# Performance work log

Measured on AMD Instinct MI355X. Metric: run time of the kernel, lower is better.

Reference implementation:

```python
import jax, jax.numpy as jnp
import numpy as np

N = 1_000_000
D = 128          # p + q, with p = q = 64
C = 1024         # number of classes
LAMBDA_LC = 1.0
LAMBDA_CC = 1.0
LAMBDA_SB = 1.0
LC_EPSILON = 0.1


def setup_inputs() -> dict:
    key = jax.random.key(0)
    k1, k2 = jax.random.split(key)
    z = jax.random.normal(k1, (N, D), dtype=jnp.float32)
    labels = jax.random.randint(k2, (N,), 0, C, dtype=jnp.int64)
    # metric vector J: +1 on first p dims, -1 on last q dims
    J = jnp.concatenate([jnp.ones(D // 2, jnp.float32), -jnp.ones(D // 2, jnp.float32)])
    return {"z": z, "labels": labels, "J": J}


def reference(z, labels, J):
    # q_J(z) = sum_d J_d z_d^2 ; shape (N,)
    q = jnp.sum(z * z * J, axis=-1)

    # light-cone penalty: mean(relu(eps - |q|))
    lc = jnp.mean(jax.nn.relu(LC_EPSILON - jnp.abs(q)))

    # causal consistency: mean over classes of within-class variance of q
    # (segment-sum form of the torch one-hot scatter; identical math)
    labels32 = labels.astype(jnp.int32)
    count = jnp.clip(jax.ops.segment_sum(jnp.ones_like(q), labels32, num_segments=C), 1.0)
    cls_mean = jax.ops.segment_sum(q, labels32, num_segments=C) / count
    sq_dev = (q - cls_mean[labels32]) ** 2
    cls_var = jax.ops.segment_sum(sq_dev, labels32, num_segments=C) / count
    cc = jnp.mean(cls_var)

    # signature balance: (mean q)^2
    sb = jnp.mean(q) ** 2

    return LAMBDA_LC * lc + LAMBDA_CC * cc + LAMBDA_SB * sb
```

## Files before the change

kernel.cpp:

```cpp
#include <hip/hip_runtime.h>

#define D_CONST 128
#define C_CONST 1024
#define LC_EPS  0.1f

#define G_HIST   512
#define TPB      1024
#define WAVES_PB (TPB / 64)
#define RED_TPB  G_HIST

#define P_OFF    0
#define LCQ_OFF  (G_HIST * 3 * C_CONST)
#define VARS_OFF (LCQ_OFF + 2 * G_HIST)
#define MAIN_WS_FLOATS (VARS_OFF + C_CONST)

__global__ __launch_bounds__(TPB) void qstat_main(const float* __restrict__ z,
                                                  const int* __restrict__ labels,
                                                  float* __restrict__ ws,
                                                  int n) {
    __shared__ float h[3 * C_CONST];
    __shared__ float wred[2 * WAVES_PB];

    for (int i = threadIdx.x; i < 3 * C_CONST; i += TPB) h[i] = 0.0f;
    __syncthreads();

    const int lane = threadIdx.x & 63;
    const int wv   = threadIdx.x >> 6;
    const int gw   = blockIdx.x * WAVES_PB + wv;
    const int nw   = G_HIST * WAVES_PB;
    const int half = lane >> 5;
    const int sub  = lane & 31;
    const float sign = (sub < 16) ? 1.0f : -1.0f;

    float lc_acc = 0.0f;
    float q_acc  = 0.0f;

    const int n_pairs = n >> 1;

    for (int base = gw * 2; base < n_pairs; base += nw * 2) {
        const int pair1 = base + 1;
        const bool has1 = pair1 < n_pairs;

        const int row0 = base * 2 + half;
        const float4 v0 = ((const float4*)(z + (long long)row0 * D_CONST))[sub];
        float4 v1;
        int row1 = 0;
        if (has1) {
            row1 = pair1 * 2 + half;
            v1 = ((const float4*)(z + (long long)row1 * D_CONST))[sub];
        }

        float s0 = (v0.x * v0.x + v0.y * v0.y + v0.z * v0.z + v0.w * v0.w) * sign;
        s0 += __shfl_xor(s0, 1);
        s0 += __shfl_xor(s0, 2);
        s0 += __shfl_xor(s0, 4);
        s0 += __shfl_xor(s0, 8);
        s0 += __shfl_xor(s0, 16);
        if (sub == 0) {
            const float q = s0;
            lc_acc += fmaxf(LC_EPS - fabsf(q), 0.0f);
            q_acc  += q;
            const int c = labels[row0];
            atomicAdd(&h[c], 1.0f);
            atomicAdd(&h[C_CONST + c], q);
            atomicAdd(&h[2 * C_CONST + c], q * q);
        }

        if (has1) {
            float s1 = (v1.x * v1.x + v1.y * v1.y + v1.z * v1.z + v1.w * v1.w) * sign;
            s1 += __shfl_xor(s1, 1);
            s1 += __shfl_xor(s1, 2);
            s1 += __shfl_xor(s1, 4);
            s1 += __shfl_xor(s1, 8);
            s1 += __shfl_xor(s1, 16);
            if (sub == 0) {
                const float q = s1;
                lc_acc += fmaxf(LC_EPS - fabsf(q), 0.0f);
                q_acc  += q;
                const int c = labels[row1];
                atomicAdd(&h[c], 1.0f);
                atomicAdd(&h[C_CONST + c], q);
                atomicAdd(&h[2 * C_CONST + c], q * q);
            }
        }
    }

    lc_acc += __shfl_xor(lc_acc, 32);
    q_acc  += __shfl_xor(q_acc, 32);
    if (lane == 0) { wred[wv] = lc_acc; wred[WAVES_PB + wv] = q_acc; }
    __syncthreads();

    if (threadIdx.x == 0) {
        float l = 0.0f, q = 0.0f;
        for (int i = 0; i < WAVES_PB; i++) { l += wred[i]; q += wred[WAVES_PB + i]; }
        ws[LCQ_OFF + blockIdx.x * 2]     = l;
        ws[LCQ_OFF + blockIdx.x * 2 + 1] = q;
    }

    float* dst = ws + P_OFF + (long long)blockIdx.x * 3 * C_CONST;
    for (int i = threadIdx.x; i < 3 * C_CONST; i += TPB) dst[i] = h[i];
}

__global__ __launch_bounds__(RED_TPB) void reduce_classes(const float* __restrict__ ws,
                                                          float* __restrict__ vars) {
    const int c = blockIdx.x;
    const int g = threadIdx.x;
    const float* p = ws + P_OFF + (long long)g * 3 * C_CONST;
    float cnt = p[c];
    float s   = p[C_CONST + c];
    float s2  = p[2 * C_CONST + c];

    for (int m = 1; m < 64; m <<= 1) {
        cnt += __shfl_xor(cnt, m);
        s   += __shfl_xor(s, m);
        s2  += __shfl_xor(s2, m);
    }
    __shared__ float r[3][RED_TPB / 64];
    const int wv = threadIdx.x >> 6;
    if ((threadIdx.x & 63) == 0) { r[0][wv] = cnt; r[1][wv] = s; r[2][wv] = s2; }
    __syncthreads();
    if (threadIdx.x == 0) {
        float C0 = 0, S0 = 0, S20 = 0;
        for (int i = 0; i < RED_TPB / 64; i++) { C0 += r[0][i]; S0 += r[1][i]; S20 += r[2][i]; }
        const float cc = fmaxf(C0, 1.0f);
        vars[c] = (S20 - S0 * S0 / cc) / cc;
    }
}

__global__ __launch_bounds__(C_CONST) void final_scalar(const float* __restrict__ ws,
                                                        float* __restrict__ out,
                                                        int n) {
    __shared__ float red[C_CONST];
    __shared__ float red2[2 * G_HIST];
    const int t = threadIdx.x;
    red[t] = ws[VARS_OFF + t];
    if (t < G_HIST) {
        red2[t]          = ws[LCQ_OFF + t * 2];
        red2[G_HIST + t] = ws[LCQ_OFF + t * 2 + 1];
    }
    __syncthreads();
    for (int off = C_CONST / 2; off > 0; off >>= 1) {
        if (t < off) red[t] += red[t + off];
        if (off <= G_HIST / 2 && t < off) {
            red2[t] += red2[t + off];
            red2[G_HIST + t] += red2[G_HIST + t + off];
        }
        __syncthreads();
    }
    if (t == 0) {
        const float lc = red2[0] / (float)n;
        const float mq = red2[G_HIST] / (float)n;
        out[0] = lc + red[0] / (float)C_CONST + mq * mq;
    }
}

#define FB_WS_FLOATS (3 * C_CONST + 2)

__global__ __launch_bounds__(256) void qstat_fb(const float* __restrict__ z,
                                                const int* __restrict__ labels,
                                                float* __restrict__ ws,
                                                int n) {
    const int lane = threadIdx.x & 63;
    const long long gw = (long long)blockIdx.x * 4 + (threadIdx.x >> 6);
    const long long nw = (long long)gridDim.x * 4;
    const int half = lane >> 5, sub = lane & 31;
    const float sign = (sub < 16) ? 1.0f : -1.0f;
    float lc = 0.0f, qa = 0.0f;
    const long long n_pairs = (long long)n >> 1;
    for (long long pair = gw; pair < n_pairs; pair += nw) {
        const long long row = pair * 2 + half;
        float4 v = ((const float4*)(z + row * D_CONST))[sub];
        float s = (v.x * v.x + v.y * v.y + v.z * v.z + v.w * v.w) * sign;
        s += __shfl_xor(s, 1); s += __shfl_xor(s, 2); s += __shfl_xor(s, 4);
        s += __shfl_xor(s, 8); s += __shfl_xor(s, 16);
        if (sub == 0) {
            lc += fmaxf(LC_EPS - fabsf(s), 0.0f); qa += s;
            const int c = labels[row];
            atomicAdd(&ws[c], 1.0f);
            atomicAdd(&ws[C_CONST + c], s);
            atomicAdd(&ws[2 * C_CONST + c], s * s);
        }
    }
    lc += __shfl_xor(lc, 32); qa += __shfl_xor(qa, 32);
    if (lane == 0) {
        atomicAdd(&ws[3 * C_CONST], lc);
        atomicAdd(&ws[3 * C_CONST + 1], qa);
    }
}

__global__ __launch_bounds__(C_CONST) void finalize_fb(const float* __restrict__ ws,
                                                       float* __restrict__ out, int n) {
    __shared__ float red[C_CONST];
    const int c = threadIdx.x;
    const float cnt = fmaxf(ws[c], 1.0f);
    const float s = ws[C_CONST + c], s2 = ws[2 * C_CONST + c];
    red[c] = (s2 - s * s / cnt) / cnt;
    __syncthreads();
    for (int off = C_CONST / 2; off > 0; off >>= 1) {
        if (c < off) red[c] += red[c + off];
        __syncthreads();
    }
    if (c == 0) {
        out[0] = ws[3 * C_CONST] / (float)n + red[0] / (float)C_CONST
               + (ws[3 * C_CONST + 1] / (float)n) * (ws[3 * C_CONST + 1] / (float)n);
    }
}

extern "C" void kernel_launch(void* const* d_in, const int* in_sizes, int n_in,
                              void* d_out, int out_size, void* d_ws, size_t ws_size,
                              hipStream_t stream) {
    const float* z      = (const float*)d_in[0];
    const int*   labels = (const int*)d_in[1];
    float* ws  = (float*)d_ws;
    float* out = (float*)d_out;
    const int n = in_sizes[1];

    if (ws_size >= (size_t)MAIN_WS_FLOATS * sizeof(float)) {
        qstat_main<<<G_HIST, TPB, 0, stream>>>(z, labels, ws, n);
        reduce_classes<<<C_CONST, RED_TPB, 0, stream>>>(ws, ws + VARS_OFF);
        final_scalar<<<1, C_CONST, 0, stream>>>(ws, out, n);
    } else {
        hipMemsetAsync(ws, 0, FB_WS_FLOATS * sizeof(float), stream);
        qstat_fb<<<2048, 256, 0, stream>>>(z, labels, ws, n);
        finalize_fb<<<1, C_CONST, 0, stream>>>(ws, out, n);
    }
}
```

Before: 665.5 us.

## Transpose partial histograms, fuse final reduction via last-block atomics, nontemporal loads

Partial per-block histograms are now stored class-major, so the class reduction kernel reads contiguous memory instead of strided, uncoalesced loads. The final scalar kernel is folded into the reduction kernel using atomic accumulation and a last-block-done counter, which removes one launch. Loads of z become nontemporal to avoid polluting the cache. The transposed store in the main kernel is now strided, and the fused finish relies on ws accumulators being zeroed by block 0 of the preceding kernel.

```diff
diff --git a/kernel.cpp b/kernel.cpp
--- a/kernel.cpp
+++ b/kernel.cpp
@@ -7,19 +7,23 @@
 #define G_HIST   512
 #define TPB      1024
 #define WAVES_PB (TPB / 64)
-#define RED_TPB  G_HIST
+#define RED_TPB  512
+
+typedef float f32x4 __attribute__((ext_vector_type(4)));
 
 #define P_OFF    0
-#define LCQ_OFF  (G_HIST * 3 * C_CONST)
-#define VARS_OFF (LCQ_OFF + 2 * G_HIST)
-#define MAIN_WS_FLOATS (VARS_OFF + C_CONST)
-
-__global__ __launch_bounds__(TPB) void qstat_main(const float* __restrict__ z,
-                                                  const int* __restrict__ labels,
-                                                  float* __restrict__ ws,
-                                                  int n) {
+#define LCQ_OFF  (3 * C_CONST * G_HIST)
+#define ACC_OFF  (LCQ_OFF + 2 * G_HIST)
+#define MAIN_WS_FLOATS (ACC_OFF + 4)
+
+__global__ __launch_bounds__(TPB, 8) void qstat_main(const float* __restrict__ z,
+                                                     const int* __restrict__ labels,
+                                                     float* __restrict__ ws,
+                                                     int n) {
     __shared__ float h[3 * C_CONST];
     __shared__ float wred[2 * WAVES_PB];
+
+    if (blockIdx.x == 0 && threadIdx.x < 4) ws[ACC_OFF + threadIdx.x] = 0.0f;
 
     for (int i = threadIdx.x; i < 3 * C_CONST; i += TPB) h[i] = 0.0f;
     __syncthreads();
@@ -42,12 +46,14 @@
         const bool has1 = pair1 < n_pairs;
 
         const int row0 = base * 2 + half;
-        const float4 v0 = ((const float4*)(z + (long long)row0 * D_CONST))[sub];
-        float4 v1;
+        const f32x4* zp0 = (const f32x4*)(z + (long long)row0 * D_CONST);
+        const f32x4 v0 = __builtin_nontemporal_load(zp0 + sub);
+        f32x4 v1;
         int row1 = 0;
         if (has1) {
             row1 = pair1 * 2 + half;
-            v1 = ((const float4*)(z + (long long)row1 * D_CONST))[sub];
+            const f32x4* zp1 = (const f32x4*)(z + (long long)row1 * D_CONST);
+            v1 = __builtin_nontemporal_load(zp1 + sub);
         }
 
         float s0 = (v0.x * v0.x + v0.y * v0.y + v0.z * v0.z + v0.w * v0.w) * sign;
@@ -93,64 +99,64 @@
     if (threadIdx.x == 0) {
         float l = 0.0f, q = 0.0f;
         for (int i = 0; i < WAVES_PB; i++) { l += wred[i]; q += wred[WAVES_PB + i]; }
-        ws[LCQ_OFF + blockIdx.x * 2]     = l;
-        ws[LCQ_OFF + blockIdx.x * 2 + 1] = q;
-    }
-
-    float* dst = ws + P_OFF + (long long)blockIdx.x * 3 * C_CONST;
-    for (int i = threadIdx.x; i < 3 * C_CONST; i += TPB) dst[i] = h[i];
-}
-
-__global__ __launch_bounds__(RED_TPB) void reduce_classes(const float* __restrict__ ws,
-                                                          float* __restrict__ vars) {
+        ws[LCQ_OFF + blockIdx.x]          = l;
+        ws[LCQ_OFF + G_HIST + blockIdx.x] = q;
+    }
+
+    for (int i = threadIdx.x; i < 3 * C_CONST; i += TPB) {
+        const int stat = i >> 10;
+        const int c    = i & (C_CONST - 1);
+        ws[P_OFF + stat * (C_CONST * G_HIST) + c * G_HIST + blockIdx.x] = h[i];
+    }
+}
+
+__global__ __launch_bounds__(RED_TPB) void reduce_final(float* __restrict__ ws,
+                                                        float* __restrict__ out,
+                                                        int n) {
     const int c = blockIdx.x;
-    const int g = threadIdx.x;
-    const float* p = ws + P_OFF + (long long)g * 3 * C_CONST;
-    float cnt = p[c];
-    float s   = p[C_CONST + c];
-    float s2  = p[2 * C_CONST + c];
+    const int t = threadIdx.x;
+    const float* p = ws + P_OFF;
+    float cnt = p[0 * C_CONST * G_HIST + c * G_HIST + t];
+    float s   = p[1 * C_CONST * G_HIST + c * G_HIST + t];
+    float s2  = p[2 * C_CONST * G_HIST + c * G_HIST + t];
+    float lcv = 0.0f, qv = 0.0f;
+    if (c == 0) {
+        lcv = ws[LCQ_OFF + t];
+        qv  = ws[LCQ_OFF + G_HIST + t];
+    }
 
     for (int m = 1; m < 64; m <<= 1) {
         cnt += __shfl_xor(cnt, m);
         s   += __shfl_xor(s, m);
         s2  += __shfl_xor(s2, m);
-    }
-    __shared__ float r[3][RED_TPB / 64];
-    const int wv = threadIdx.x >> 6;
-    if ((threadIdx.x & 63) == 0) { r[0][wv] = cnt; r[1][wv] = s; r[2][wv] = s2; }
-    __syncthreads();
-    if (threadIdx.x == 0) {
-        float C0 = 0, S0 = 0, S20 = 0;
-        for (int i = 0; i < RED_TPB / 64; i++) { C0 += r[0][i]; S0 += r[1][i]; S20 += r[2][i]; }
+        lcv += __shfl_xor(lcv, m);
+        qv  += __shfl_xor(qv, m);
+    }
+    __shared__ float r[5][RED_TPB / 64];
+    const int wv = t >> 6;
+    if ((t & 63) == 0) { r[0][wv] = cnt; r[1][wv] = s; r[2][wv] = s2;
+                         r[3][wv] = lcv; r[4][wv] = qv; }
+    __syncthreads();
+    if (t == 0) {
+        float C0 = 0, S0 = 0, S20 = 0, L0 = 0, Q0 = 0;
+        for (int i = 0; i < RED_TPB / 64; i++) {
+            C0 += r[0][i]; S0 += r[1][i]; S20 += r[2][i]; L0 += r[3][i]; Q0 += r[4][i];
+        }
         const float cc = fmaxf(C0, 1.0f);
-        vars[c] = (S20 - S0 * S0 / cc) / cc;
-    }
-}
-
-__global__ __launch_bounds__(C_CONST) void final_scalar(const float* __restrict__ ws,
-                                                        float* __restrict__ out,
-                                                        int n) {
-    __shared__ float red[C_CONST];
-    __shared__ float red2[2 * G_HIST];
-    const int t = threadIdx.x;
-    red[t] = ws[VARS_OFF + t];
-    if (t < G_HIST) {
-        red2[t]          = ws[LCQ_OFF + t * 2];
-        red2[G_HIST + t] = ws[LCQ_OFF + t * 2 + 1];
-    }
-    __syncthreads();
-    for (int off = C_CONST / 2; off > 0; off >>= 1) {
-        if (t < off) red[t] += red[t + off];
-        if (off <= G_HIST / 2 && t < off) {
-            red2[t] += red2[t + off];
-            red2[G_HIST + t] += red2[G_HIST + t + off];
-        }
-        __syncthreads();
-    }
-    if (t == 0) {
-        const float lc = red2[0] / (float)n;
-        const float mq = red2[G_HIST] / (float)n;
-        out[0] = lc + red[0] / (float)C_CONST + mq * mq;
+        atomicAdd(&ws[ACC_OFF + 0], (S20 - S0 * S0 / cc) / cc);
+        if (c == 0) {
+            atomicAdd(&ws[ACC_OFF + 1], L0);
+            atomicAdd(&ws[ACC_OFF + 2], Q0);
+        }
+        __threadfence();
+        const int old = atomicAdd((int*)(ws + ACC_OFF + 3), 1);
+        if (old == C_CONST - 1) {
+            const float v = atomicAdd(&ws[ACC_OFF + 0], 0.0f);
+            const float l = atomicAdd(&ws[ACC_OFF + 1], 0.0f);
+            const float q = atomicAdd(&ws[ACC_OFF + 2], 0.0f);
+            const float mq = q / (float)n;
+            out[0] = l / (float)n + v / (float)C_CONST + mq * mq;
+        }
     }
 }
 
@@ -217,8 +223,7 @@
 
     if (ws_size >= (size_t)MAIN_WS_FLOATS * sizeof(float)) {
         qstat_main<<<G_HIST, TPB, 0, stream>>>(z, labels, ws, n);
-        reduce_classes<<<C_CONST, RED_TPB, 0, stream>>>(ws, ws + VARS_OFF);
-        final_scalar<<<1, C_CONST, 0, stream>>>(ws, out, n);
+        reduce_final<<<C_CONST, RED_TPB, 0, stream>>>(ws, out, n);
     } else {
         hipMemsetAsync(ws, 0, FB_WS_FLOATS * sizeof(float), stream);
         qstat_fb<<<2048, 256, 0, stream>>>(z, labels, ws, n);
```

Result: no change. 675.5 us (+1.5%).

## Merge per-block histograms with global atomics and drop the class-reduction kernel

Applied to the files above, without the earlier changes.

Each block now adds its shared-memory class histogram and its lc/q partial sums straight into one global accumulator using atomics, after a memset. This replaces the 512-way per-block partial buffer, the reduce_classes kernel and final_scalar. It also hoists the label loads ahead of the shuffle reductions and adds a minimum-blocks hint to launch_bounds. The aim is to cut the partial-buffer write and reread and one kernel launch, at the cost of heavy global atomic contention on 3072 addresses and a float summation order that is no longer deterministic.

```diff
diff --git a/kernel.cpp b/kernel.cpp
--- a/kernel.cpp
+++ b/kernel.cpp
@@ -7,17 +7,13 @@
 #define G_HIST   512
 #define TPB      1024
 #define WAVES_PB (TPB / 64)
-#define RED_TPB  G_HIST
 
-#define P_OFF    0
-#define LCQ_OFF  (G_HIST * 3 * C_CONST)
-#define VARS_OFF (LCQ_OFF + 2 * G_HIST)
-#define MAIN_WS_FLOATS (VARS_OFF + C_CONST)
+#define WS_FLOATS (3 * C_CONST + 2)
 
-__global__ __launch_bounds__(TPB) void qstat_main(const float* __restrict__ z,
-                                                  const int* __restrict__ labels,
-                                                  float* __restrict__ ws,
-                                                  int n) {
+__global__ __launch_bounds__(TPB, 8) void qstat_main(const float* __restrict__ z,
+                                                     const int* __restrict__ labels,
+                                                     float* __restrict__ ws,
+                                                     int n) {
     __shared__ float h[3 * C_CONST];
     __shared__ float wred[2 * WAVES_PB];
 
@@ -50,6 +46,12 @@
             v1 = ((const float4*)(z + (long long)row1 * D_CONST))[sub];
         }
 
+        int c0 = 0, c1 = 0;
+        if (sub == 0) {
+            c0 = labels[row0];
+            if (has1) c1 = labels[row1];
+        }
+
         float s0 = (v0.x * v0.x + v0.y * v0.y + v0.z * v0.z + v0.w * v0.w) * sign;
         s0 += __shfl_xor(s0, 1);
         s0 += __shfl_xor(s0, 2);
@@ -60,10 +62,9 @@
             const float q = s0;
             lc_acc += fmaxf(LC_EPS - fabsf(q), 0.0f);
             q_acc  += q;
-            const int c = labels[row0];
-            atomicAdd(&h[c], 1.0f);
-            atomicAdd(&h[C_CONST + c], q);
-            atomicAdd(&h[2 * C_CONST + c], q * q);
+            atomicAdd(&h[c0], 1.0f);
+            atomicAdd(&h[C_CONST + c0], q);
+            atomicAdd(&h[2 * C_CONST + c0], q * q);
         }
 
         if (has1) {
@@ -77,10 +78,9 @@
                 const float q = s1;
                 lc_acc += fmaxf(LC_EPS - fabsf(q), 0.0f);
                 q_acc  += q;
-                const int c = labels[row1];
-                atomicAdd(&h[c], 1.0f);
-                atomicAdd(&h[C_CONST + c], q);
-                atomicAdd(&h[2 * C_CONST + c], q * q);
+                atomicAdd(&h[c1], 1.0f);
+                atomicAdd(&h[C_CONST + c1], q);
+                atomicAdd(&h[2 * C_CONST + c1], q * q);
             }
         }
     }
@@ -93,107 +93,23 @@
     if (threadIdx.x == 0) {
         float l = 0.0f, q = 0.0f;
         for (int i = 0; i < WAVES_PB; i++) { l += wred[i]; q += wred[WAVES_PB + i]; }
-        ws[LCQ_OFF + blockIdx.x * 2]     = l;
-        ws[LCQ_OFF + blockIdx.x * 2 + 1] = q;
+        atomicAdd(&ws[3 * C_CONST], l);
+        atomicAdd(&ws[3 * C_CONST + 1], q);
     }
 
-    float* dst = ws + P_OFF + (long long)blockIdx.x * 3 * C_CONST;
-    for (int i = threadIdx.x; i < 3 * C_CONST; i += TPB) dst[i] = h[i];
-}
-
-__global__ __launch_bounds__(RED_TPB) void reduce_classes(const float* __restrict__ ws,
-                                                          float* __restrict__ vars) {
-    const int c = blockIdx.x;
-    const int g = threadIdx.x;
-    const float* p = ws + P_OFF + (long long)g * 3 * C_CONST;
-    float cnt = p[c];
-    float s   = p[C_CONST + c];
-    float s2  = p[2 * C_CONST + c];
-
-    for (int m = 1; m < 64; m <<= 1) {
-        cnt += __shfl_xor(cnt, m);
-        s   += __shfl_xor(s, m);
-        s2  += __shfl_xor(s2, m);
-    }
-    __shared__ float r[3][RED_TPB / 64];
-    const int wv = threadIdx.x >> 6;
-    if ((threadIdx.x & 63) == 0) { r[0][wv] = cnt; r[1][wv] = s; r[2][wv] = s2; }
-    __syncthreads();
-    if (threadIdx.x == 0) {
-        float C0 = 0, S0 = 0, S20 = 0;
-        for (int i = 0; i < RED_TPB / 64; i++) { C0 += r[0][i]; S0 += r[1][i]; S20 += r[2][i]; }
-        const float cc = fmaxf(C0, 1.0f);
-        vars[c] = (S20 - S0 * S0 / cc) / cc;
+    for (int i = threadIdx.x; i < 3 * C_CONST; i += TPB) {
+        atomicAdd(&ws[i], h[i]);
     }
 }
 
-__global__ __launch_bounds__(C_CONST) void final_scalar(const float* __restrict__ ws,
-                                                        float* __restrict__ out,
-                                                        int n) {
-    __shared__ float red[C_CONST];
-    __shared__ float red2[2 * G_HIST];
-    const int t = threadIdx.x;
-    red[t] = ws[VARS_OFF + t];
-    if (t < G_HIST) {
-        red2[t]          = ws[LCQ_OFF + t * 2];
-        red2[G_HIST + t] = ws[LCQ_OFF + t * 2 + 1];
-    }
-    __syncthreads();
-    for (int off = C_CONST / 2; off > 0; off >>= 1) {
-        if (t < off) red[t] += red[t + off];
-        if (off <= G_HIST / 2 && t < off) {
-            red2[t] += red2[t + off];
-            red2[G_HIST + t] += red2[G_HIST + t + off];
-        }
-        __syncthreads();
-    }
-    if (t == 0) {
-        const float lc = red2[0] / (float)n;
-        const float mq = red2[G_HIST] / (float)n;
-        out[0] = lc + red[0] / (float)C_CONST + mq * mq;
-    }
-}
-
-#define FB_WS_FLOATS (3 * C_CONST + 2)
-
-__global__ __launch_bounds__(256) void qstat_fb(const float* __restrict__ z,
-                                                const int* __restrict__ labels,
-                                                float* __restrict__ ws,
-                                                int n) {
-    const int lane = threadIdx.x & 63;
-    const long long gw = (long long)blockIdx.x * 4 + (threadIdx.x >> 6);
-    const long long nw = (long long)gridDim.x * 4;
-    const int half = lane >> 5, sub = lane & 31;
-    const float sign = (sub < 16) ? 1.0f : -1.0f;
-    float lc = 0.0f, qa = 0.0f;
-    const long long n_pairs = (long long)n >> 1;
-    for (long long pair = gw; pair < n_pairs; pair += nw) {
-        const long long row = pair * 2 + half;
-        float4 v = ((const float4*)(z + row * D_CONST))[sub];
-        float s = (v.x * v.x + v.y * v.y + v.z * v.z + v.w * v.w) * sign;
-        s += __shfl_xor(s, 1); s += __shfl_xor(s, 2); s += __shfl_xor(s, 4);
-        s += __shfl_xor(s, 8); s += __shfl_xor(s, 16);
-        if (sub == 0) {
-            lc += fmaxf(LC_EPS - fabsf(s), 0.0f); qa += s;
-            const int c = labels[row];
-            atomicAdd(&ws[c], 1.0f);
-            atomicAdd(&ws[C_CONST + c], s);
-            atomicAdd(&ws[2 * C_CONST + c], s * s);
-        }
-    }
-    lc += __shfl_xor(lc, 32); qa += __shfl_xor(qa, 32);
-    if (lane == 0) {
-        atomicAdd(&ws[3 * C_CONST], lc);
-        atomicAdd(&ws[3 * C_CONST + 1], qa);
-    }
-}
-
-__global__ __launch_bounds__(C_CONST) void finalize_fb(const float* __restrict__ ws,
-                                                       float* __restrict__ out, int n) {
+__global__ __launch_bounds__(C_CONST) void finalize_main(const float* __restrict__ ws,
+                                                         float* __restrict__ out,
+                                                         int n) {
     __shared__ float red[C_CONST];
     const int c = threadIdx.x;
     const float cnt = fmaxf(ws[c], 1.0f);
-    const float s = ws[C_CONST + c], s2 = ws[2 * C_CONST + c];
+    const float s   = ws[C_CONST + c];
+    const float s2  = ws[2 * C_CONST + c];
     red[c] = (s2 - s * s / cnt) / cnt;
     __syncthreads();
     for (int off = C_CONST / 2; off > 0; off >>= 1) {
@@ -201,8 +117,9 @@
         __syncthreads();
     }
     if (c == 0) {
-        out[0] = ws[3 * C_CONST] / (float)n + red[0] / (float)C_CONST
-               + (ws[3 * C_CONST + 1] / (float)n) * (ws[3 * C_CONST + 1] / (float)n);
+        const float lc = ws[3 * C_CONST] / (float)n;
+        const float mq = ws[3 * C_CONST + 1] / (float)n;
+        out[0] = lc + red[0] / (float)C_CONST + mq * mq;
     }
 }
 
@@ -215,13 +132,7 @@
     float* out = (float*)d_out;
     const int n = in_sizes[1];
 
-    if (ws_size >= (size_t)MAIN_WS_FLOATS * sizeof(float)) {
-        qstat_main<<<G_HIST, TPB, 0, stream>>>(z, labels, ws, n);
-        reduce_classes<<<C_CONST, RED_TPB, 0, stream>>>(ws, ws + VARS_OFF);
-        final_scalar<<<1, C_CONST, 0, stream>>>(ws, out, n);
-    } else {
-        hipMemsetAsync(ws, 0, FB_WS_FLOATS * sizeof(float), stream);
-        qstat_fb<<<2048, 256, 0, stream>>>(z, labels, ws, n);
-        finalize_fb<<<1, C_CONST, 0, stream>>>(ws, out, n);
-    }
+    hipMemsetAsync(ws, 0, WS_FLOATS * sizeof(float), stream);
+    qstat_main<<<G_HIST, TPB, 0, stream>>>(z, labels, ws, n);
+    finalize_main<<<1, C_CONST, 0, stream>>>(ws, out, n);
 }
```

After: 653.7 us. About the same (-1.8%).
